# Performance work log

Measured on AMD Instinct MI355X. Metric: run time of the kernel, lower is better.

The kernel has to match this reference:

```python
import jax, jax.numpy as jnp
import numpy as np

EMBED_DIM = 1024
MEMORY_SIZE = 64
TOPK = 3
LN_EPS = 1e-5


def setup_inputs() -> dict:
    key = jax.random.key(0)
    ks = jax.random.split(key, 8)
    D, M = EMBED_DIM, MEMORY_SIZE
    scale = 1.0 / np.sqrt(D)
    x = jax.random.normal(ks[0], (8, 2048, D), dtype=jnp.float32)
    memory = jax.random.normal(ks[1], (M, D), dtype=jnp.float32) * scale
    Wq = jax.random.normal(ks[2], (D, D), dtype=jnp.float32) * scale
    bq = jnp.zeros((D,), dtype=jnp.float32)
    Wf = jax.random.normal(ks[3], (D, 2 * D), dtype=jnp.float32) * (1.0 / np.sqrt(2 * D))
    bf = jnp.zeros((D,), dtype=jnp.float32)
    gamma = jnp.ones((D,), dtype=jnp.float32)
    beta = jnp.zeros((D,), dtype=jnp.float32)
    return {"x": x, "memory": memory, "Wq": Wq, "bq": bq,
            "Wf": Wf, "bf": bf, "gamma": gamma, "beta": beta}


def reference(x, memory, Wq, bq, Wf, bf, gamma, beta):
    B, S, D = x.shape
    # query projection: [B,S,D]
    query = jnp.einsum('bsd,ed->bse', x, Wq) + bq
    # similarity to memory bank: [B,S,M]
    sim = jnp.einsum('bsd,md->bsm', query, memory)
    # top-k over memory slots
    topk_sim, topk_idx = jax.lax.top_k(sim, TOPK)            # [B,S,K]
    weights = jax.nn.softmax(topk_sim, axis=-1)               # [B,S,K]
    retrieved = memory[topk_idx]                              # [B,S,K,D]
    memory_output = jnp.einsum('bskd,bsk->bsd', retrieved, weights)
    # fusion MLP: Linear(2D->D) -> LayerNorm -> ReLU
    cat = jnp.concatenate([x, memory_output], axis=-1)        # [B,S,2D]
    h = jnp.einsum('bsc,dc->bsd', cat, Wf) + bf
    mean = jnp.mean(h, axis=-1, keepdims=True)
    var = jnp.mean(jnp.square(h - mean), axis=-1, keepdims=True)
    h = (h - mean) * jax.lax.rsqrt(var + LN_EPS) * gamma + beta
    return jax.nn.relu(h)
```

## Files before the change

kernel.cpp:

```cpp
#include <hip/hip_runtime.h>

#define DCH 1024
#define MSLOT 64
#define NTOK 16384

typedef __bf16 bf16x8 __attribute__((ext_vector_type(8)));
typedef float f32x4 __attribute__((ext_vector_type(4)));
typedef unsigned short u16x8 __attribute__((ext_vector_type(8)));
typedef unsigned short u16x4 __attribute__((ext_vector_type(4)));

__device__ __forceinline__ unsigned short f2bf(float f) {
  unsigned u = __float_as_uint(f);
  u += 0x7fffu + ((u >> 16) & 1u);
  return (unsigned short)(u >> 16);
}
__device__ __forceinline__ float bf2f(unsigned short s) {
  return __uint_as_float(((unsigned)s) << 16);
}

__device__ __forceinline__ void gld16(const void* g, void* l) {
  __builtin_amdgcn_global_load_lds((const __attribute__((address_space(1))) void*)g,
                                   (__attribute__((address_space(3))) void*)l, 16, 0, 0);
}

__global__ __launch_bounds__(256) void prep_a_kernel(
    const float* __restrict__ x, unsigned short* __restrict__ xb,
    const float* __restrict__ Wf, float* __restrict__ Wf2T,
    unsigned short* __restrict__ Wf1b,
    const float* __restrict__ bq, const float* __restrict__ memv,
    float* __restrict__ sc) {
  __shared__ float tile[64][65];
  __shared__ float red[256];
  const int b = blockIdx.x, tid = threadIdx.x;

  if (b < 8192) {
    int idx8 = (b * 256 + tid) * 8;
    float4 a = *(const float4*)(x + idx8);
    float4 c = *(const float4*)(x + idx8 + 4);
    u16x8 o = {f2bf(a.x), f2bf(a.y), f2bf(a.z), f2bf(a.w),
               f2bf(c.x), f2bf(c.y), f2bf(c.z), f2bf(c.w)};
    *(u16x8*)(xb + idx8) = o;
  } else if (b < 8448) {
    const int t = b - 8192;
    const int c0 = (t & 15) * 64, d0 = (t >> 4) * 64;
    const int lane = tid & 63, wv = tid >> 6;
#pragma unroll
    for (int i = 0; i < 16; ++i) {
      int r = wv + i * 4;
      tile[r][lane] = Wf[(size_t)(d0 + r) * 2048 + 1024 + c0 + lane];
    }
    __syncthreads();
#pragma unroll
    for (int i = 0; i < 16; ++i) {
      int r = wv + i * 4;
      Wf2T[(size_t)(c0 + r) * 1024 + d0 + lane] = tile[lane][r];
    }
  } else if (b < 8512) {
    const int j = b - 8448;
#pragma unroll
    for (int i = 0; i < 16; ++i) {
      int f4 = j * 4096 + i * 256 + tid;
      int row = f4 >> 8, c4 = (f4 & 255) * 4;
      float4 v = *(const float4*)(Wf + (size_t)row * 2048 + c4);
      u16x4 o = {f2bf(v.x), f2bf(v.y), f2bf(v.z), f2bf(v.w)};
      *(u16x4*)(Wf1b + row * 1024 + c4) = o;
    }
  } else {
    int m = tid >> 2, q = tid & 3;
    float s = 0.f;
    for (int e = q * 256; e < q * 256 + 256; ++e) s += bq[e] * memv[m * 1024 + e];
    red[tid] = s;
    __syncthreads();
    if (tid < 64) sc[tid] = red[tid * 4] + red[tid * 4 + 1] + red[tid * 4 + 2] + red[tid * 4 + 3];
  }
}

__global__ __launch_bounds__(256) void prep_b_kernel(
    const float* __restrict__ memv, const float* __restrict__ Wq,
    const float* __restrict__ Wf2T,
    float* __restrict__ partWm, float* __restrict__ partP) {
  int b = blockIdx.x;
  const int tid = threadIdx.x;
  const int which = b >> 7;
  b &= 127;
  const int kc = b & 7, dt = (b >> 3) & 3, mg = b >> 5;
  const float* B = which ? Wf2T : Wq;
  float* outp = which ? partP : partWm;
  const int d = dt * 256 + tid;
  const int e0 = kc * 128;
  const int m0 = mg * 16;

  float acc[16];
#pragma unroll
  for (int m = 0; m < 16; ++m) acc[m] = 0.f;

  const float* bp = B + (size_t)e0 * 1024 + d;
  const float* mp = memv + m0 * 1024 + e0;
#pragma unroll 4
  for (int e = 0; e < 128; ++e) {
    float wv = bp[(size_t)e * 1024];
#pragma unroll
    for (int m = 0; m < 16; ++m) acc[m] += mp[m * 1024 + e] * wv;
  }
  float* op = outp + ((size_t)kc * 64 + m0) * 1024 + d;
#pragma unroll
  for (int m = 0; m < 16; ++m) op[m * 1024] = acc[m];
}

__global__ __launch_bounds__(256) void prep_c_kernel(
    const float* __restrict__ partWm, const float* __restrict__ partP,
    unsigned short* __restrict__ Wmb, float* __restrict__ P) {
  int idx = blockIdx.x * 256 + threadIdx.x;
  if (idx < 65536) {
    float s = 0.f;
#pragma unroll
    for (int k = 0; k < 8; ++k) s += partWm[k * 65536 + idx];
    Wmb[idx] = f2bf(s);
  } else {
    idx -= 65536;
    float s = 0.f;
#pragma unroll
    for (int k = 0; k < 8; ++k) s += partP[k * 65536 + idx];
    P[idx] = s;
  }
}

__global__ __launch_bounds__(256) void sim_topk_kernel(
    const unsigned short* __restrict__ xb, const unsigned short* __restrict__ Wmb,
    const float* __restrict__ sc, float4* __restrict__ meta) {
  __shared__ __attribute__((aligned(16))) unsigned short As[64 * 64];
  __shared__ __attribute__((aligned(16))) unsigned short Bs[64 * 64];
  __shared__ float sim_s[64 * 65];
  const int tid = threadIdx.x;
  const int wave = tid >> 6, lane = tid & 63;
  const int tok0 = blockIdx.x * 64;
  const int quad = lane >> 4, cl = lane & 15;

  f32x4 acc[4];
#pragma unroll
  for (int j = 0; j < 4; ++j) acc[j] = {0.f, 0.f, 0.f, 0.f};

  for (int kt = 0; kt < 16; ++kt) {
    __syncthreads();
#pragma unroll
    for (int i = 0; i < 2; ++i) {
      int ch = (wave * 2 + i) * 64 + lane;
      int row = ch >> 3, cb = (ch & 7) * 8;
      gld16(xb + (size_t)(tok0 + row) * 1024 + kt * 64 + cb, As + ch * 8);
      gld16(Wmb + row * 1024 + kt * 64 + cb, Bs + ch * 8);
    }
    __syncthreads();
    const unsigned short* Ab = As + (wave * 16 + cl) * 64 + quad * 8;
    const unsigned short* Bb = Bs + cl * 64 + quad * 8;
#pragma unroll
    for (int ks = 0; ks < 2; ++ks) {
      bf16x8 a = *(const bf16x8*)(Ab + ks * 32);
#pragma unroll
      for (int nt = 0; nt < 4; ++nt) {
        bf16x8 bb = *(const bf16x8*)(Bb + nt * 16 * 64 + ks * 32);
        acc[nt] = __builtin_amdgcn_mfma_f32_16x16x32_bf16(a, bb, acc[nt], 0, 0, 0);
      }
    }
  }
#pragma unroll
  for (int nt = 0; nt < 4; ++nt)
#pragma unroll
    for (int r = 0; r < 4; ++r) {
      int lt = wave * 16 + quad * 4 + r;
      int mc = nt * 16 + cl;
      sim_s[lt * 65 + mc] = acc[nt][r] + sc[mc];
    }
  __syncthreads();
  if (tid < 64) {
    const float* sp = sim_s + tid * 65;
    float s0 = -1e30f, s1 = -1e30f, s2 = -1e30f;
    int i0 = 0, i1 = 0, i2 = 0;
    for (int m = 0; m < 64; ++m) {
      float v = sp[m];
      if (v > s0) { s2 = s1; i2 = i1; s1 = s0; i1 = i0; s0 = v; i0 = m; }
      else if (v > s1) { s2 = s1; i2 = i1; s1 = v; i1 = m; }
      else if (v > s2) { s2 = v; i2 = m; }
    }
    float e1 = __expf(s1 - s0), e2 = __expf(s2 - s0);
    float inv = 1.f / (1.f + e1 + e2);
    meta[tok0 + tid] = make_float4(inv, e1 * inv, e2 * inv,
                                   __int_as_float(i0 | (i1 << 8) | (i2 << 16)));
  }
}

__global__ __launch_bounds__(256, 2) void gemm_h_kernel(
    const unsigned short* __restrict__ xb, const unsigned short* __restrict__ Wf1b,
    unsigned short* __restrict__ hb) {
  __shared__ __attribute__((aligned(16))) unsigned short As[256 * 64];
  __shared__ __attribute__((aligned(16))) unsigned short Bs[128 * 64];
  const int tid = threadIdx.x;
  const int wave = tid >> 6, lane = tid & 63;
  const int b = blockIdx.x;
  const int tok0 = (b & 63) * 256, d0 = (b >> 6) * 128;
  const int quad = lane >> 4, cl = lane & 15;
  const int wm = wave * 64;

  f32x4 acc[4][8];
#pragma unroll
  for (int i = 0; i < 4; ++i)
#pragma unroll
    for (int j = 0; j < 8; ++j) acc[i][j] = {0.f, 0.f, 0.f, 0.f};

  for (int kt = 0; kt < 16; ++kt) {
    __syncthreads();
#pragma unroll
    for (int i = 0; i < 8; ++i) {
      int ch = (wave * 8 + i) * 64 + lane;
      int row = ch >> 3, cb = (ch & 7) * 8;
      gld16(xb + (size_t)(tok0 + row) * 1024 + kt * 64 + cb, As + ch * 8);
    }
#pragma unroll
    for (int i = 0; i < 4; ++i) {
      int ch = (wave * 4 + i) * 64 + lane;
      int row = ch >> 3, cb = (ch & 7) * 8;
      gld16(Wf1b + (size_t)(d0 + row) * 1024 + kt * 64 + cb, Bs + ch * 8);
    }
    __syncthreads();
    const unsigned short* Ab = As + (wm + cl) * 64 + quad * 8;
    const unsigned short* Bb = Bs + cl * 64 + quad * 8;
#pragma unroll
    for (int ks = 0; ks < 2; ++ks) {
      bf16x8 a[4], bb[8];
#pragma unroll
      for (int t = 0; t < 4; ++t) a[t] = *(const bf16x8*)(Ab + t * 1024 + ks * 32);
#pragma unroll
      for (int t = 0; t < 8; ++t) bb[t] = *(const bf16x8*)(Bb + t * 1024 + ks * 32);
#pragma unroll
      for (int mt = 0; mt < 4; ++mt)
#pragma unroll
        for (int nt = 0; nt < 8; ++nt)
          acc[mt][nt] = __builtin_amdgcn_mfma_f32_16x16x32_bf16(a[mt], bb[nt], acc[mt][nt], 0, 0, 0);
    }
  }

#pragma unroll
  for (int mt = 0; mt < 4; ++mt) {
#pragma unroll
    for (int r = 0; r < 4; ++r) {
      int row = tok0 + wm + mt * 16 + quad * 4 + r;
#pragma unroll
      for (int nt = 0; nt < 8; ++nt) {
        int d = d0 + nt * 16 + cl;
        hb[(size_t)row * 1024 + d] = f2bf(acc[mt][nt][r]);
      }
    }
  }
}

__global__ __launch_bounds__(256) void ln_relu_kernel(
    const unsigned short* __restrict__ hb, const float* __restrict__ P,
    const float4* __restrict__ meta, const float* __restrict__ bfv,
    const float* __restrict__ gamma, const float* __restrict__ beta,
    float* __restrict__ out) {
  const int tid = threadIdx.x;
  const int wave = tid >> 6, lane = tid & 63;
  const int t = blockIdx.x * 4 + wave;
  const int dbase = lane * 16;

  float4 mv = meta[t];
  int pk = __float_as_int(mv.w);
  const float* P0 = P + (pk & 255) * 1024 + dbase;
  const float* P1 = P + ((pk >> 8) & 255) * 1024 + dbase;
  const float* P2 = P + ((pk >> 16) & 255) * 1024 + dbase;
  const float* bp = bfv + dbase;

  const unsigned short* hp = hb + (size_t)t * 1024 + dbase;
  u16x8 h0 = *(const u16x8*)(hp);
  u16x8 h1 = *(const u16x8*)(hp + 8);
  float f[16];
#pragma unroll
  for (int j = 0; j < 8; ++j) { f[j] = bf2f(h0[j]); f[8 + j] = bf2f(h1[j]); }
#pragma unroll
  for (int j4 = 0; j4 < 4; ++j4) {
    float4 b4 = *(const float4*)(bp + j4 * 4);
    float4 p0 = *(const float4*)(P0 + j4 * 4);
    float4 p1 = *(const float4*)(P1 + j4 * 4);
    float4 p2 = *(const float4*)(P2 + j4 * 4);
    f[j4 * 4 + 0] += b4.x + mv.x * p0.x + mv.y * p1.x + mv.z * p2.x;
    f[j4 * 4 + 1] += b4.y + mv.x * p0.y + mv.y * p1.y + mv.z * p2.y;
    f[j4 * 4 + 2] += b4.z + mv.x * p0.z + mv.y * p1.z + mv.z * p2.z;
    f[j4 * 4 + 3] += b4.w + mv.x * p0.w + mv.y * p1.w + mv.z * p2.w;
  }
  float s = 0.f, q = 0.f;
#pragma unroll
  for (int j = 0; j < 16; ++j) { s += f[j]; q += f[j] * f[j]; }
#pragma unroll
  for (int off = 32; off; off >>= 1) {
    s += __shfl_xor(s, off);
    q += __shfl_xor(q, off);
  }
  float mean = s * (1.f / 1024.f);
  float var = q * (1.f / 1024.f) - mean * mean;
  float rs = rsqrtf(var + 1e-5f);
  float o[16];
#pragma unroll
  for (int j = 0; j < 16; ++j) {
    float v = (f[j] - mean) * rs * gamma[dbase + j] + beta[dbase + j];
    o[j] = fmaxf(v, 0.f);
  }
  float* op = out + (size_t)t * 1024 + dbase;
#pragma unroll
  for (int j4 = 0; j4 < 4; ++j4) {
    float4 v = {o[j4 * 4], o[j4 * 4 + 1], o[j4 * 4 + 2], o[j4 * 4 + 3]};
    *(float4*)(op + j4 * 4) = v;
  }
}

extern "C" void kernel_launch(void* const* d_in, const int* in_sizes, int n_in,
                              void* d_out, int out_size, void* d_ws, size_t ws_size,
                              hipStream_t stream) {
  const float* x     = (const float*)d_in[0];
  const float* memv  = (const float*)d_in[1];
  const float* Wq    = (const float*)d_in[2];
  const float* bq    = (const float*)d_in[3];
  const float* Wf    = (const float*)d_in[4];
  const float* bfv   = (const float*)d_in[5];
  const float* gamma = (const float*)d_in[6];
  const float* beta  = (const float*)d_in[7];
  float* out = (float*)d_out;
  char* ws = (char*)d_ws;

  unsigned short* Wf1b   = (unsigned short*)(ws);
  unsigned short* Wmb    = (unsigned short*)(ws + 2097152);
  float*          P      = (float*)(ws + 2228224);
  float*          sc     = (float*)(ws + 2490368);
  float4*         meta   = (float4*)(ws + 2490624);
  float*          Wf2T   = (float*)(ws + 2752768);
  float*          partWm = (float*)(ws + 6947072);
  float*          partP  = (float*)(ws + 9044224);
  unsigned short* xb     = (unsigned short*)(ws + 11141376);
  unsigned short* hb     = (unsigned short*)(ws + 44695808);

  hipLaunchKernelGGL(prep_a_kernel, dim3(8513), dim3(256), 0, stream,
                     x, xb, Wf, Wf2T, Wf1b, bq, memv, sc);
  hipLaunchKernelGGL(prep_b_kernel, dim3(256), dim3(256), 0, stream,
                     memv, Wq, Wf2T, partWm, partP);
  hipLaunchKernelGGL(prep_c_kernel, dim3(512), dim3(256), 0, stream,
                     partWm, partP, Wmb, P);
  hipLaunchKernelGGL(sim_topk_kernel, dim3(256), dim3(256), 0, stream,
                     xb, Wmb, sc, meta);
  hipLaunchKernelGGL(gemm_h_kernel, dim3(512), dim3(256), 0, stream,
                     xb, Wf1b, hb);
  hipLaunchKernelGGL(ln_relu_kernel, dim3(4096), dim3(256), 0, stream,
                     hb, P, meta, bfv, gamma, beta, out);
}
```

Before: 267.0 us.

## Swizzle LDS tiles in GEMM kernels, narrow x cast, vectorize LN params

```diff
diff --git a/kernel.cpp b/kernel.cpp
--- a/kernel.cpp
+++ b/kernel.cpp
@@ -33,15 +33,13 @@
   __shared__ float red[256];
   const int b = blockIdx.x, tid = threadIdx.x;
 
-  if (b < 8192) {
-    int idx8 = (b * 256 + tid) * 8;
-    float4 a = *(const float4*)(x + idx8);
-    float4 c = *(const float4*)(x + idx8 + 4);
-    u16x8 o = {f2bf(a.x), f2bf(a.y), f2bf(a.z), f2bf(a.w),
-               f2bf(c.x), f2bf(c.y), f2bf(c.z), f2bf(c.w)};
-    *(u16x8*)(xb + idx8) = o;
-  } else if (b < 8448) {
-    const int t = b - 8192;
+  if (b < 16384) {
+    int idx4 = (b * 256 + tid) * 4;
+    float4 a = *(const float4*)(x + idx4);
+    u16x4 o = {f2bf(a.x), f2bf(a.y), f2bf(a.z), f2bf(a.w)};
+    *(u16x4*)(xb + idx4) = o;
+  } else if (b < 16640) {
+    const int t = b - 16384;
     const int c0 = (t & 15) * 64, d0 = (t >> 4) * 64;
     const int lane = tid & 63, wv = tid >> 6;
 #pragma unroll
@@ -55,8 +53,8 @@
       int r = wv + i * 4;
       Wf2T[(size_t)(c0 + r) * 1024 + d0 + lane] = tile[lane][r];
     }
-  } else if (b < 8512) {
-    const int j = b - 8448;
+  } else if (b < 16704) {
+    const int j = b - 16640;
 #pragma unroll
     for (int i = 0; i < 16; ++i) {
       int f4 = j * 4096 + i * 256 + tid;
@@ -135,6 +133,9 @@
   const int wave = tid >> 6, lane = tid & 63;
   const int tok0 = blockIdx.x * 64;
   const int quad = lane >> 4, cl = lane & 15;
+  const int sw = ((lane & 7) ^ (lane >> 3)) * 8;
+  const int cx0 = ((quad) ^ (cl & 7)) * 8;
+  const int cx1 = ((quad + 4) ^ (cl & 7)) * 8;
 
   f32x4 acc[4];
 #pragma unroll
@@ -145,19 +146,18 @@
 #pragma unroll
     for (int i = 0; i < 2; ++i) {
       int ch = (wave * 2 + i) * 64 + lane;
-      int row = ch >> 3, cb = (ch & 7) * 8;
-      gld16(xb + (size_t)(tok0 + row) * 1024 + kt * 64 + cb, As + ch * 8);
-      gld16(Wmb + row * 1024 + kt * 64 + cb, Bs + ch * 8);
-    }
-    __syncthreads();
-    const unsigned short* Ab = As + (wave * 16 + cl) * 64 + quad * 8;
-    const unsigned short* Bb = Bs + cl * 64 + quad * 8;
+      int row = ch >> 3;
+      gld16(xb + (size_t)(tok0 + row) * 1024 + kt * 64 + sw, As + ch * 8);
+      gld16(Wmb + row * 1024 + kt * 64 + sw, Bs + ch * 8);
+    }
+    __syncthreads();
 #pragma unroll
     for (int ks = 0; ks < 2; ++ks) {
-      bf16x8 a = *(const bf16x8*)(Ab + ks * 32);
+      const int cx = ks ? cx1 : cx0;
+      bf16x8 a = *(const bf16x8*)(As + (wave * 16 + cl) * 64 + cx);
 #pragma unroll
       for (int nt = 0; nt < 4; ++nt) {
-        bf16x8 bb = *(const bf16x8*)(Bb + nt * 16 * 64 + ks * 32);
+        bf16x8 bb = *(const bf16x8*)(Bs + (cl + nt * 16) * 64 + cx);
         acc[nt] = __builtin_amdgcn_mfma_f32_16x16x32_bf16(a, bb, acc[nt], 0, 0, 0);
       }
     }
@@ -199,6 +199,9 @@
   const int tok0 = (b & 63) * 256, d0 = (b >> 6) * 128;
   const int quad = lane >> 4, cl = lane & 15;
   const int wm = wave * 64;
+  const int sw = ((lane & 7) ^ (lane >> 3)) * 8;
+  const int cx0 = ((quad) ^ (cl & 7)) * 8;
+  const int cx1 = ((quad + 4) ^ (cl & 7)) * 8;
 
   f32x4 acc[4][8];
 #pragma unroll
@@ -211,25 +214,26 @@
 #pragma unroll
     for (int i = 0; i < 8; ++i) {
       int ch = (wave * 8 + i) * 64 + lane;
-      int row = ch >> 3, cb = (ch & 7) * 8;
-      gld16(xb + (size_t)(tok0 + row) * 1024 + kt * 64 + cb, As + ch * 8);
+      int row = ch >> 3;
+      gld16(xb + (size_t)(tok0 + row) * 1024 + kt * 64 + sw, As + ch * 8);
     }
 #pragma unroll
     for (int i = 0; i < 4; ++i) {
       int ch = (wave * 4 + i) * 64 + lane;
-      int row = ch >> 3, cb = (ch & 7) * 8;
-      gld16(Wf1b + (size_t)(d0 + row) * 1024 + kt * 64 + cb, Bs + ch * 8);
-    }
-    __syncthreads();
-    const unsigned short* Ab = As + (wm + cl) * 64 + quad * 8;
-    const unsigned short* Bb = Bs + cl * 64 + quad * 8;
+      int row = ch >> 3;
+      gld16(Wf1b + (size_t)(d0 + row) * 1024 + kt * 64 + sw, Bs + ch * 8);
+    }
+    __syncthreads();
 #pragma unroll
     for (int ks = 0; ks < 2; ++ks) {
+      const int cx = ks ? cx1 : cx0;
       bf16x8 a[4], bb[8];
 #pragma unroll
-      for (int t = 0; t < 4; ++t) a[t] = *(const bf16x8*)(Ab + t * 1024 + ks * 32);
-#pragma unroll
-      for (int t = 0; t < 8; ++t) bb[t] = *(const bf16x8*)(Bb + t * 1024 + ks * 32);
+      for (int t = 0; t < 4; ++t)
+        a[t] = *(const bf16x8*)(As + (wm + cl + t * 16) * 64 + cx);
+#pragma unroll
+      for (int t = 0; t < 8; ++t)
+        bb[t] = *(const bf16x8*)(Bs + (cl + t * 16) * 64 + cx);
 #pragma unroll
       for (int mt = 0; mt < 4; ++mt)
 #pragma unroll
@@ -297,16 +301,16 @@
   float mean = s * (1.f / 1024.f);
   float var = q * (1.f / 1024.f) - mean * mean;
   float rs = rsqrtf(var + 1e-5f);
-  float o[16];
-#pragma unroll
-  for (int j = 0; j < 16; ++j) {
-    float v = (f[j] - mean) * rs * gamma[dbase + j] + beta[dbase + j];
-    o[j] = fmaxf(v, 0.f);
-  }
   float* op = out + (size_t)t * 1024 + dbase;
 #pragma unroll
   for (int j4 = 0; j4 < 4; ++j4) {
-    float4 v = {o[j4 * 4], o[j4 * 4 + 1], o[j4 * 4 + 2], o[j4 * 4 + 3]};
+    float4 g4 = *(const float4*)(gamma + dbase + j4 * 4);
+    float4 e4 = *(const float4*)(beta + dbase + j4 * 4);
+    float4 v;
+    v.x = fmaxf((f[j4 * 4 + 0] - mean) * rs * g4.x + e4.x, 0.f);
+    v.y = fmaxf((f[j4 * 4 + 1] - mean) * rs * g4.y + e4.y, 0.f);
+    v.z = fmaxf((f[j4 * 4 + 2] - mean) * rs * g4.z + e4.z, 0.f);
+    v.w = fmaxf((f[j4 * 4 + 3] - mean) * rs * g4.w + e4.w, 0.f);
     *(float4*)(op + j4 * 4) = v;
   }
 }
@@ -336,7 +340,7 @@
   unsigned short* xb     = (unsigned short*)(ws + 11141376);
   unsigned short* hb     = (unsigned short*)(ws + 44695808);
 
-  hipLaunchKernelGGL(prep_a_kernel, dim3(8513), dim3(256), 0, stream,
+  hipLaunchKernelGGL(prep_a_kernel, dim3(16705), dim3(256), 0, stream,
                      x, xb, Wf, Wf2T, Wf1b, bq, memv, sc);
   hipLaunchKernelGGL(prep_b_kernel, dim3(256), dim3(256), 0, stream,
                      memv, Wq, Wf2T, partWm, partP);
```

Result: faster. 259.3 us (-2.9%).
